# Kernel tuning notes

Hardware: AMD Instinct MI355X
Metric: run time of the kernel (lower is better)

Reference implementation:

```python
import jax, jax.numpy as jnp
import numpy as np


def conv1x1(x, w, b):
    # x: [B,Ci,H,W], w: [Co,Ci,1,1], b: [Co]
    return jnp.einsum('bihw,oi->bohw', x, w[:, :, 0, 0]) + b[None, :, None, None]


def guide_nn(x, w1, b1, w2, b2):
    h = jax.nn.relu(conv1x1(x, w1, b1))
    return jnp.tanh(conv1x1(h, w2, b2))


def trilinear_slice(grid, gx, gy, gz):
    # grid: [B,C,D,Gh,Gw]; gx,gy,gz: [B,H,W] in ~[-1,1]
    B, C, D, Gh, Gw = grid.shape
    fx = jnp.clip((gx + 1.0) * 0.5 * (Gw - 1), 0.0, Gw - 1)
    fy = jnp.clip((gy + 1.0) * 0.5 * (Gh - 1), 0.0, Gh - 1)
    fz = jnp.clip((gz + 1.0) * 0.5 * (D - 1), 0.0, D - 1)
    x0 = jnp.floor(fx).astype(jnp.int32); x1 = jnp.minimum(x0 + 1, Gw - 1)
    y0 = jnp.floor(fy).astype(jnp.int32); y1 = jnp.minimum(y0 + 1, Gh - 1)
    z0 = jnp.floor(fz).astype(jnp.int32); z1 = jnp.minimum(z0 + 1, D - 1)
    wx = (fx - x0)[:, None]; wy = (fy - y0)[:, None]; wz = (fz - z0)[:, None]

    gather = jax.vmap(lambda g, zi, yi, xi: g[:, zi, yi, xi])  # -> [B,C,H,W]

    out = (
        gather(grid, z0, y0, x0) * (1 - wz) * (1 - wy) * (1 - wx)
        + gather(grid, z0, y0, x1) * (1 - wz) * (1 - wy) * wx
        + gather(grid, z0, y1, x0) * (1 - wz) * wy * (1 - wx)
        + gather(grid, z0, y1, x1) * (1 - wz) * wy * wx
        + gather(grid, z1, y0, x0) * wz * (1 - wy) * (1 - wx)
        + gather(grid, z1, y0, x1) * wz * (1 - wy) * wx
        + gather(grid, z1, y1, x0) * wz * wy * (1 - wx)
        + gather(grid, z1, y1, x1) * wz * wy * wx
    )
    return out


def slicing(grid, guide):
    # guide: [B,1,H,W] (single-channel context map)
    B, c, H, W = guide.shape
    x = (jnp.arange(W, dtype=guide.dtype) - W / 2) / (W / 2)
    y = (jnp.arange(H, dtype=guide.dtype) - H / 2) / (H / 2)
    yy, xx = jnp.meshgrid(y, x, indexing='ij')
    gx = jnp.broadcast_to(xx[None], (B, H, W))
    gy = jnp.broadcast_to(yy[None], (B, H, W))
    gz = guide[:, 0]
    return trilinear_slice(grid, gx, gy, gz)


def apply_coefficent(x, coeff):
    # x: [B,Ci,H,W]; coeff: [B,Co,Ci+1,H,W] -> per-pixel affine
    ci = x.shape[1]
    return jnp.einsum('boihw,bihw->bohw', coeff[:, :, :ci], x) + coeff[:, :, ci]


def setup_inputs() -> dict:
    key = jax.random.key(0)
    ks = jax.random.split(key, 12)
    B, H, W = 8, 512, 512
    D, Gh, Gw = 8, 16, 16
    inp = {
        'src': jax.random.uniform(ks[0], (B, 3, H, W), jnp.float32),
        'grid1': jax.random.normal(ks[1], (B, 32, D, Gh, Gw), jnp.float32),
        'grid2': jax.random.normal(ks[2], (B, 27, D, Gh, Gw), jnp.float32),
        'w1': jax.random.normal(ks[3], (16, 3, 1, 1), jnp.float32) * 0.1,
        'b1': jnp.zeros((16,), jnp.float32),
        'w2': jax.random.normal(ks[4], (1, 16, 1, 1), jnp.float32) * 0.1,
        'b2': jnp.zeros((1,), jnp.float32),
        'w3': jax.random.normal(ks[5], (16, 8, 1, 1), jnp.float32) * 0.1,
        'b3': jnp.zeros((16,), jnp.float32),
        'w4': jax.random.normal(ks[6], (1, 16, 1, 1), jnp.float32) * 0.1,
        'b4': jnp.zeros((1,), jnp.float32),
    }
    return inp


def reference(src, grid1, grid2, w1, b1, w2, b2, w3, b3, w4, b4):
    B, _, H, W = src.shape
    context_map = guide_nn(src, w1, b1, w2, b2)            # [B,1,H,W]
    coeff1 = slicing(grid1, context_map)                    # [B,32,H,W]
    coeff1_split = jnp.transpose(coeff1.reshape(B, 4, 8, H, W), (0, 2, 1, 3, 4))  # [B,8,4,H,W]
    hidden = jax.nn.relu(apply_coefficent(src, coeff1_split))  # [B,8,H,W]
    context_map2 = guide_nn(hidden, w3, b3, w4, b4)         # [B,1,H,W]
    coeff2 = slicing(grid2, context_map2)                   # [B,27,H,W]
    coeff2_split = jnp.transpose(coeff2.reshape(B, 9, 3, H, W), (0, 2, 1, 3, 4))  # [B,3,9,H,W]
    out = apply_coefficent(hidden, coeff2_split)            # [B,3,H,W]
    return out
```

## Files before the change

### kernel.cpp

```cpp
#include <hip/hip_runtime.h>
#include <math.h>

#define BATCH 8
#define IMH 512
#define IMW 512
#define HWSZ (IMH * IMW)
#define CH 32
#define CPADH 40
#define L_CELLS (16 * 8)
#define LSLOTH (L_CELLS * CPADH)

typedef _Float16 h1;
typedef _Float16 h2 __attribute__((ext_vector_type(2)));

union V16 {
    uint4 u;
    h2 h[4];
};
union V8 {
    uint2 u;
    h2 h[2];
};

__device__ __forceinline__ float fast_tanh(float x) {
    float e = __expf(2.0f * x);
    return fmaf(-2.0f, __builtin_amdgcn_rcpf(e + 1.0f), 1.0f);
}
__device__ __forceinline__ unsigned packh(float a, float b) {
    h2 v;
    v[0] = (h1)a;
    v[1] = (h1)b;
    return __builtin_bit_cast(unsigned, v);
}
__device__ __forceinline__ h2 ash2(unsigned u) { return __builtin_bit_cast(h2, u); }
__device__ __forceinline__ h2 pkmax0(h2 v) { return __builtin_elementwise_max(v, (h2)(h1)0.0f); }


__global__ __launch_bounds__(256) void transpose_both(const float* __restrict__ g1,
                                                      const float* __restrict__ g2,
                                                      h1* __restrict__ t1,
                                                      h1* __restrict__ t2,
                                                      unsigned* __restrict__ wpk,
                                                      const float* __restrict__ w1,
                                                      const float* __restrict__ b1,
                                                      const float* __restrict__ w2,
                                                      const float* __restrict__ w3,
                                                      const float* __restrict__ b3,
                                                      const float* __restrict__ w4) {
    int idx = blockIdx.x * 256 + threadIdx.x;
    if (idx < 524288) {
        int x = idx & 15, y = (idx >> 4) & 15, z = (idx >> 8) & 7;
        int c = (idx >> 11) & 31, b = idx >> 16;
        t1[((((b * 16 + y) * 16 + x) * 8 + z) << 5) + c] = (h1)g1[idx];
    } else if (idx < 966656) {
        int j = idx - 524288;
        int x = j & 15, y = (j >> 4) & 15, z = (j >> 8) & 7;
        int r = j >> 11;
        int c = r % 27, b = r / 27;
        t2[((((b * 16 + y) * 16 + x) * 8 + z) << 5) + c] = (h1)g2[j];
    } else {
        int k = idx - 966656;
        int cell = k / 5, p = k - cell * 5;
        t2[(cell << 5) + 27 + p] = (h1)0.0f;
    }
    if (blockIdx.x == 4095) {
        int t = threadIdx.x;
        if (t < 24) {
            int i = t >> 3, n = t & 7;
            wpk[t] = packh(w1[2 * n * 3 + i], w1[(2 * n + 1) * 3 + i]);
        } else if (t < 32) {
            int n = t - 24;
            wpk[t] = packh(b1[2 * n], b1[2 * n + 1]);
        } else if (t < 40) {
            int n = t - 32;
            wpk[t] = packh(w2[2 * n], w2[2 * n + 1]);
        } else if (t < 104) {
            int k = t - 40;
            int n = k >> 3, i = k & 7;
            wpk[t] = packh(w3[2 * n * 8 + i], w3[(2 * n + 1) * 8 + i]);
        } else if (t < 112) {
            int n = t - 104;
            wpk[t] = packh(w4[2 * n], w4[2 * n + 1]);
        } else if (t < 120) {
            int n = t - 112;
            wpk[t] = packh(b3[2 * n], b3[2 * n + 1]);
        }
    }
}

template <bool TR>
__global__ __launch_bounds__(512, 8) void fused9(
    const float* __restrict__ src,
    const void* __restrict__ g1p,
    const void* __restrict__ g2p,
    const unsigned* __restrict__ wpk,
    const float* __restrict__ w1, const float* __restrict__ b1,
    const float* __restrict__ w2, const float* __restrict__ b2,
    const float* __restrict__ w3, const float* __restrict__ b3,
    const float* __restrict__ w4, const float* __restrict__ b4,
    float* __restrict__ out) {
    __shared__ __align__(16) h1 L1h[LSLOTH];
    __shared__ __align__(16) h1 L2h[LSLOTH];

    int tid = threadIdx.x;
    int h = blockIdx.x & 511;
    int b = blockIdx.x >> 9;

    float fy = (float)h * (15.0f / 512.0f);
    int y0 = (int)fy;
    float wy = fy - (float)y0;

    const float* sbase = src + (size_t)b * 3 * HWSZ + (size_t)h * IMW;
    float s0 = sbase[tid];
    float s1 = sbase[HWSZ + tid];
    float s2 = sbase[2 * HWSZ + tid];

    if (TR) {
        h2 wyh = (h2)(h1)wy;
        const uint4* p1 = (const uint4*)g1p + ((size_t)b * 16 + y0) * 512;
        const uint4* p2 = (const uint4*)g2p + ((size_t)b * 16 + y0) * 512;
        int g = tid & 3, cell = tid >> 2;
        V16 v0, v1, r0;
        v0.u = p1[tid];
        v1.u = p1[tid + 512];
#pragma unroll
        for (int k = 0; k < 4; ++k) r0.h[k] = v0.h[k] + (v1.h[k] - v0.h[k]) * wyh;
        *(uint4*)&L1h[cell * CPADH + 8 * g] = r0.u;
        V16 u0, u1, r1;
        u0.u = p2[tid];
        u1.u = p2[tid + 512];
#pragma unroll
        for (int k = 0; k < 4; ++k) r1.h[k] = u0.h[k] + (u1.h[k] - u0.h[k]) * wyh;
        *(uint4*)&L2h[cell * CPADH + 8 * g] = r1.u;
    } else {
        const float* g1f = (const float*)g1p;
        const float* g2f = (const float*)g2p;
        for (int t = tid; t < L_CELLS * CH; t += 512) {
            int c = t & 31, cell = t >> 5;
            int z = cell & 7, xj = cell >> 3;
            size_t o0 = ((((size_t)b * 32 + c) * 8 + z) * 16 + y0) * 16 + xj;
            float v0 = g1f[o0], v1 = g1f[o0 + 16];
            L1h[cell * CPADH + c] = (h1)fmaf(wy, v1 - v0, v0);
        }
        for (int t = tid; t < L_CELLS * CH; t += 512) {
            int c = t & 31, cell = t >> 5;
            int z = cell & 7, xj = cell >> 3;
            float v = 0.0f;
            if (c < 27) {
                size_t o0 = ((((size_t)b * 27 + c) * 8 + z) * 16 + y0) * 16 + xj;
                v = fmaf(wy, g2f[o0 + 16] - g2f[o0], g2f[o0]);
            }
            L2h[cell * CPADH + c] = (h1)v;
        }
    }
    __syncthreads();

    float* obase = out + (size_t)b * 3 * HWSZ + (size_t)h * IMW;
    int w = tid;

    float acc;
    h2 s0h, s1h, s2h;
    if constexpr (TR) {
        s0h = (h2)(h1)s0;
        s1h = (h2)(h1)s1;
        s2h = (h2)(h1)s2;
        h2 A;
#pragma unroll
        for (int n = 0; n < 8; ++n) {
            h2 t = ash2(wpk[24 + n]);
            t += s0h * ash2(wpk[n]);
            t += s1h * ash2(wpk[8 + n]);
            t += s2h * ash2(wpk[16 + n]);
            t = pkmax0(t);
            if (n == 0) A = t * ash2(wpk[32]);
            else        A += t * ash2(wpk[32 + n]);
        }
        acc = b2[0] + (float)A[0] + (float)A[1];
    } else {
        acc = b2[0];
#pragma unroll
        for (int j = 0; j < 16; ++j) {
            float t = fmaf(w1[j * 3 + 0], s0,
                      fmaf(w1[j * 3 + 1], s1,
                      fmaf(w1[j * 3 + 2], s2, b1[j])));
            acc = fmaf(w2[j], fmaxf(t, 0.0f), acc);
        }
    }
    float fz = fmaf(fast_tanh(acc), 3.5f, 3.5f);
    fz = fminf(fmaxf(fz, 0.0f), 7.0f);
    int z0 = min((int)fz, 6);
    float wz = fz - (float)z0;

    float fx = (float)w * (15.0f / 512.0f);
    int x0 = (int)fx;
    float wx = fx - (float)x0;
    int a00 = (x0 * 8 + z0) * CPADH;

    float w11v = wx * wz;
    float w10v = wx - w11v;
    float w01v = wz - w11v;
    float w00v = 1.0f - wx - wz + w11v;
    h2 W00 = (h2)(h1)w00v, W01 = (h2)(h1)w01v, W10 = (h2)(h1)w10v, W11 = (h2)(h1)w11v;

    const uint4* p00 = (const uint4*)&L1h[a00];
    const uint4* p01 = (const uint4*)&L1h[a00 + CPADH];
    const uint4* p10 = (const uint4*)&L1h[a00 + 8 * CPADH];
    const uint4* p11 = (const uint4*)&L1h[a00 + 9 * CPADH];
    h2 c1h[16];
#pragma unroll
    for (int j = 0; j < 4; ++j) {
        V16 A, B, C, D;
        A.u = p00[j];
        B.u = p01[j];
        C.u = p10[j];
        D.u = p11[j];
#pragma unroll
        for (int k = 0; k < 4; ++k)
            c1h[j * 4 + k] = A.h[k] * W00 + B.h[k] * W01 + C.h[k] * W10 + D.h[k] * W11;
    }

    h2 hidh[4];
    float hidf[8];
    if constexpr (TR) {
#pragma unroll
        for (int n = 0; n < 4; ++n) {
            h2 t = c1h[12 + n];
            t += c1h[n] * s0h;
            t += c1h[4 + n] * s1h;
            t += c1h[8 + n] * s2h;
            hidh[n] = pkmax0(t);
        }
    } else {
#pragma unroll
        for (int o = 0; o < 8; ++o) {
            float t = fmaf((float)c1h[o >> 1][o & 1], s0,
                      fmaf((float)c1h[(8 + o) >> 1][o & 1], s1,
                      fmaf((float)c1h[(16 + o) >> 1][o & 1], s2,
                           (float)c1h[(24 + o) >> 1][o & 1])));
            hidf[o] = fmaxf(t, 0.0f);
        }
    }

    float acc2;
    if constexpr (TR) {
        h2 hs[8];
#pragma unroll
        for (int n = 0; n < 4; ++n) {
            hs[2 * n]     = (h2)hidh[n][0];
            hs[2 * n + 1] = (h2)hidh[n][1];
        }
        h2 A;
#pragma unroll
        for (int n = 0; n < 8; ++n) {
            h2 t = ash2(wpk[112 + n]);
#pragma unroll
            for (int i = 0; i < 8; ++i) t += hs[i] * ash2(wpk[40 + n * 8 + i]);
            t = pkmax0(t);
            if (n == 0) A = t * ash2(wpk[104]);
            else        A += t * ash2(wpk[104 + n]);
        }
        acc2 = b4[0] + (float)A[0] + (float)A[1];
#pragma unroll
        for (int n = 0; n < 4; ++n) {
            hidf[2 * n]     = (float)hidh[n][0];
            hidf[2 * n + 1] = (float)hidh[n][1];
        }
    } else {
        acc2 = b4[0];
#pragma unroll
        for (int j = 0; j < 16; ++j) {
            float t = b3[j];
#pragma unroll
            for (int i = 0; i < 8; ++i) t = fmaf(w3[j * 8 + i], hidf[i], t);
            acc2 = fmaf(w4[j], fmaxf(t, 0.0f), acc2);
        }
    }
    float fz2 = fmaf(fast_tanh(acc2), 3.5f, 3.5f);
    fz2 = fminf(fmaxf(fz2, 0.0f), 7.0f);
    int z0b = min((int)fz2, 6);
    float wz2 = fz2 - (float)z0b;

    int a00b = (x0 * 8 + z0b) * CPADH;
    float u11 = wx * wz2;
    float u10 = wx - u11;
    float u01 = wz2 - u11;
    float u00 = 1.0f - wx - wz2 + u11;
    h2 U00 = (h2)(h1)u00, U01 = (h2)(h1)u01, U10 = (h2)(h1)u10, U11 = (h2)(h1)u11;

    const uint4* q00 = (const uint4*)&L2h[a00b];
    const uint4* q01 = (const uint4*)&L2h[a00b + CPADH];
    const uint4* q10 = (const uint4*)&L2h[a00b + 8 * CPADH];
    const uint4* q11 = (const uint4*)&L2h[a00b + 9 * CPADH];
    h2 c2h[14];
#pragma unroll
    for (int j = 0; j < 3; ++j) {
        V16 A, B, C, D;
        A.u = q00[j];
        B.u = q01[j];
        C.u = q10[j];
        D.u = q11[j];
#pragma unroll
        for (int k = 0; k < 4; ++k)
            c2h[j * 4 + k] = A.h[k] * U00 + B.h[k] * U01 + C.h[k] * U10 + D.h[k] * U11;
    }
    {
        V8 A, B, C, D;
        A.u = *(const uint2*)&L2h[a00b + 24];
        B.u = *(const uint2*)&L2h[a00b + CPADH + 24];
        C.u = *(const uint2*)&L2h[a00b + 8 * CPADH + 24];
        D.u = *(const uint2*)&L2h[a00b + 9 * CPADH + 24];
#pragma unroll
        for (int k = 0; k < 2; ++k)
            c2h[12 + k] = A.h[k] * U00 + B.h[k] * U01 + C.h[k] * U10 + D.h[k] * U11;
    }

#pragma unroll
    for (int o = 0; o < 3; ++o) {
        float t = (float)c2h[(24 + o) >> 1][(24 + o) & 1];
#pragma unroll
        for (int i = 0; i < 8; ++i) {
            int c = i * 3 + o;
            t = fmaf((float)c2h[c >> 1][c & 1], hidf[i], t);
        }
        obase[(size_t)o * HWSZ + w] = t;
    }
}

extern "C" void kernel_launch(void* const* d_in, const int* in_sizes, int n_in,
                              void* d_out, int out_size, void* d_ws, size_t ws_size,
                              hipStream_t stream) {
    const float* src   = (const float*)d_in[0];
    const float* grid1 = (const float*)d_in[1];
    const float* grid2 = (const float*)d_in[2];
    const float* w1 = (const float*)d_in[3];
    const float* b1 = (const float*)d_in[4];
    const float* w2 = (const float*)d_in[5];
    const float* b2 = (const float*)d_in[6];
    const float* w3 = (const float*)d_in[7];
    const float* b3 = (const float*)d_in[8];
    const float* w4 = (const float*)d_in[9];
    const float* b4 = (const float*)d_in[10];
    float* out = (float*)d_out;

    const size_t t_elems = (size_t)BATCH * 2048 * CH;
    const size_t ws_needed = 2 * t_elems * sizeof(h1) + 512;

    const int nblk = BATCH * IMH;

    if (ws_size >= ws_needed) {
        h1* t1 = (h1*)d_ws;
        h1* t2 = t1 + t_elems;
        unsigned* wpk = (unsigned*)(t2 + t_elems);
        transpose_both<<<4096, 256, 0, stream>>>(grid1, grid2, t1, t2, wpk,
                                                 w1, b1, w2, w3, b3, w4);
        fused9<true><<<nblk, 512, 0, stream>>>(
            src, t1, t2, wpk, w1, b1, w2, b2, w3, b3, w4, b4, out);
    } else {
        fused9<false><<<nblk, 512, 0, stream>>>(
            src, grid1, grid2, nullptr, w1, b1, w2, b2, w3, b3, w4, b4, out);
    }
}
```

Measured before the change: 119.7 us.

## Process four rows per block with double-buffered LDS slabs and prefetch

Each block now handles four consecutive image rows instead of one, cutting the grid to a quarter of its former size. Grid-slab loads and the next row's source pixels are issued before the current row is computed, so global-load latency can overlap with compute, and the slab goes into an alternating LDS buffer. This removes per-block launch and prologue cost and the separate load-then-sync stall for each row. In exchange it doubles shared-memory use, lowers the occupancy hint from 8 to 6, keeps more prefetched values in registers, and leaves fewer blocks to spread across CUs.

```diff
diff --git a/kernel.cpp b/kernel.cpp
--- a/kernel.cpp
+++ b/kernel.cpp
@@ -9,6 +9,7 @@
 #define CPADH 40
 #define L_CELLS (16 * 8)
 #define LSLOTH (L_CELLS * CPADH)
+#define ROWS 4
 
 typedef _Float16 h1;
 typedef _Float16 h2 __attribute__((ext_vector_type(2)));
@@ -89,7 +90,7 @@
 }
 
 template <bool TR>
-__global__ __launch_bounds__(512, 8) void fused9(
+__global__ __launch_bounds__(512, 6) void fused10(
     const float* __restrict__ src,
     const void* __restrict__ g1p,
     const void* __restrict__ g2p,
@@ -99,230 +100,279 @@
     const float* __restrict__ w3, const float* __restrict__ b3,
     const float* __restrict__ w4, const float* __restrict__ b4,
     float* __restrict__ out) {
-    __shared__ __align__(16) h1 L1h[LSLOTH];
-    __shared__ __align__(16) h1 L2h[LSLOTH];
+    __shared__ __align__(16) h1 L1h[2][LSLOTH];
+    __shared__ __align__(16) h1 L2h[2][LSLOTH];
 
     int tid = threadIdx.x;
-    int h = blockIdx.x & 511;
-    int b = blockIdx.x >> 9;
-
-    float fy = (float)h * (15.0f / 512.0f);
-    int y0 = (int)fy;
-    float wy = fy - (float)y0;
-
-    const float* sbase = src + (size_t)b * 3 * HWSZ + (size_t)h * IMW;
-    float s0 = sbase[tid];
-    float s1 = sbase[HWSZ + tid];
-    float s2 = sbase[2 * HWSZ + tid];
-
-    if (TR) {
-        h2 wyh = (h2)(h1)wy;
-        const uint4* p1 = (const uint4*)g1p + ((size_t)b * 16 + y0) * 512;
-        const uint4* p2 = (const uint4*)g2p + ((size_t)b * 16 + y0) * 512;
-        int g = tid & 3, cell = tid >> 2;
+    int b = blockIdx.x >> 7;
+    int h0 = (blockIdx.x & 127) << 2;
+
+    const float* sb0 = src + (size_t)b * 3 * HWSZ;
+    float* ob0 = out + (size_t)b * 3 * HWSZ;
+    int g = tid & 3, cell = tid >> 2;
+
+    uint4 va, vb, ua, ub;
+    float s0c, s1c, s2c, s0n, s1n, s2n;
+
+    auto issue_loads = [&](int r) {
+        float fyr = (float)(h0 + r) * (15.0f / 512.0f);
+        int y0r = (int)fyr;
+        const uint4* p1 = (const uint4*)g1p + ((size_t)b * 16 + y0r) * 512;
+        const uint4* p2 = (const uint4*)g2p + ((size_t)b * 16 + y0r) * 512;
+        va = p1[tid];
+        vb = p1[tid + 512];
+        ua = p2[tid];
+        ub = p2[tid + 512];
+    };
+    auto write_slab = [&](int r, int bi) {
+        float fyr = (float)(h0 + r) * (15.0f / 512.0f);
+        int y0r = (int)fyr;
+        h2 wyh = (h2)(h1)(fyr - (float)y0r);
         V16 v0, v1, r0;
-        v0.u = p1[tid];
-        v1.u = p1[tid + 512];
+        v0.u = va;
+        v1.u = vb;
 #pragma unroll
         for (int k = 0; k < 4; ++k) r0.h[k] = v0.h[k] + (v1.h[k] - v0.h[k]) * wyh;
-        *(uint4*)&L1h[cell * CPADH + 8 * g] = r0.u;
+        *(uint4*)&L1h[bi][cell * CPADH + 8 * g] = r0.u;
         V16 u0, u1, r1;
-        u0.u = p2[tid];
-        u1.u = p2[tid + 512];
+        u0.u = ua;
+        u1.u = ub;
 #pragma unroll
         for (int k = 0; k < 4; ++k) r1.h[k] = u0.h[k] + (u1.h[k] - u0.h[k]) * wyh;
-        *(uint4*)&L2h[cell * CPADH + 8 * g] = r1.u;
-    } else {
-        const float* g1f = (const float*)g1p;
-        const float* g2f = (const float*)g2p;
-        for (int t = tid; t < L_CELLS * CH; t += 512) {
-            int c = t & 31, cell = t >> 5;
-            int z = cell & 7, xj = cell >> 3;
-            size_t o0 = ((((size_t)b * 32 + c) * 8 + z) * 16 + y0) * 16 + xj;
-            float v0 = g1f[o0], v1 = g1f[o0 + 16];
-            L1h[cell * CPADH + c] = (h1)fmaf(wy, v1 - v0, v0);
-        }
-        for (int t = tid; t < L_CELLS * CH; t += 512) {
-            int c = t & 31, cell = t >> 5;
-            int z = cell & 7, xj = cell >> 3;
-            float v = 0.0f;
-            if (c < 27) {
-                size_t o0 = ((((size_t)b * 27 + c) * 8 + z) * 16 + y0) * 16 + xj;
-                v = fmaf(wy, g2f[o0 + 16] - g2f[o0], g2f[o0]);
-            }
-            L2h[cell * CPADH + c] = (h1)v;
-        }
+        *(uint4*)&L2h[bi][cell * CPADH + 8 * g] = r1.u;
+    };
+
+    if constexpr (TR) {
+        const float* sb = sb0 + (size_t)h0 * IMW;
+        s0c = sb[tid];
+        s1c = sb[HWSZ + tid];
+        s2c = sb[2 * HWSZ + tid];
+        issue_loads(0);
+        write_slab(0, 0);
     }
-    __syncthreads();
-
-    float* obase = out + (size_t)b * 3 * HWSZ + (size_t)h * IMW;
-    int w = tid;
-
-    float acc;
-    h2 s0h, s1h, s2h;
-    if constexpr (TR) {
-        s0h = (h2)(h1)s0;
-        s1h = (h2)(h1)s1;
-        s2h = (h2)(h1)s2;
-        h2 A;
-#pragma unroll
-        for (int n = 0; n < 8; ++n) {
-            h2 t = ash2(wpk[24 + n]);
-            t += s0h * ash2(wpk[n]);
-            t += s1h * ash2(wpk[8 + n]);
-            t += s2h * ash2(wpk[16 + n]);
-            t = pkmax0(t);
-            if (n == 0) A = t * ash2(wpk[32]);
-            else        A += t * ash2(wpk[32 + n]);
-        }
-        acc = b2[0] + (float)A[0] + (float)A[1];
-    } else {
-        acc = b2[0];
-#pragma unroll
-        for (int j = 0; j < 16; ++j) {
-            float t = fmaf(w1[j * 3 + 0], s0,
-                      fmaf(w1[j * 3 + 1], s1,
-                      fmaf(w1[j * 3 + 2], s2, b1[j])));
-            acc = fmaf(w2[j], fmaxf(t, 0.0f), acc);
-        }
-    }
-    float fz = fmaf(fast_tanh(acc), 3.5f, 3.5f);
-    fz = fminf(fmaxf(fz, 0.0f), 7.0f);
-    int z0 = min((int)fz, 6);
-    float wz = fz - (float)z0;
-
-    float fx = (float)w * (15.0f / 512.0f);
-    int x0 = (int)fx;
-    float wx = fx - (float)x0;
-    int a00 = (x0 * 8 + z0) * CPADH;
-
-    float w11v = wx * wz;
-    float w10v = wx - w11v;
-    float w01v = wz - w11v;
-    float w00v = 1.0f - wx - wz + w11v;
-    h2 W00 = (h2)(h1)w00v, W01 = (h2)(h1)w01v, W10 = (h2)(h1)w10v, W11 = (h2)(h1)w11v;
-
-    const uint4* p00 = (const uint4*)&L1h[a00];
-    const uint4* p01 = (const uint4*)&L1h[a00 + CPADH];
-    const uint4* p10 = (const uint4*)&L1h[a00 + 8 * CPADH];
-    const uint4* p11 = (const uint4*)&L1h[a00 + 9 * CPADH];
-    h2 c1h[16];
-#pragma unroll
-    for (int j = 0; j < 4; ++j) {
-        V16 A, B, C, D;
-        A.u = p00[j];
-        B.u = p01[j];
-        C.u = p10[j];
-        D.u = p11[j];
-#pragma unroll
-        for (int k = 0; k < 4; ++k)
-            c1h[j * 4 + k] = A.h[k] * W00 + B.h[k] * W01 + C.h[k] * W10 + D.h[k] * W11;
-    }
-
-    h2 hidh[4];
-    float hidf[8];
-    if constexpr (TR) {
-#pragma unroll
-        for (int n = 0; n < 4; ++n) {
-            h2 t = c1h[12 + n];
-            t += c1h[n] * s0h;
-            t += c1h[4 + n] * s1h;
-            t += c1h[8 + n] * s2h;
-            hidh[n] = pkmax0(t);
-        }
-    } else {
-#pragma unroll
-        for (int o = 0; o < 8; ++o) {
-            float t = fmaf((float)c1h[o >> 1][o & 1], s0,
-                      fmaf((float)c1h[(8 + o) >> 1][o & 1], s1,
-                      fmaf((float)c1h[(16 + o) >> 1][o & 1], s2,
-                           (float)c1h[(24 + o) >> 1][o & 1])));
-            hidf[o] = fmaxf(t, 0.0f);
-        }
-    }
-
-    float acc2;
-    if constexpr (TR) {
-        h2 hs[8];
-#pragma unroll
-        for (int n = 0; n < 4; ++n) {
-            hs[2 * n]     = (h2)hidh[n][0];
-            hs[2 * n + 1] = (h2)hidh[n][1];
-        }
-        h2 A;
-#pragma unroll
-        for (int n = 0; n < 8; ++n) {
-            h2 t = ash2(wpk[112 + n]);
-#pragma unroll
-            for (int i = 0; i < 8; ++i) t += hs[i] * ash2(wpk[40 + n * 8 + i]);
-            t = pkmax0(t);
-            if (n == 0) A = t * ash2(wpk[104]);
-            else        A += t * ash2(wpk[104 + n]);
-        }
-        acc2 = b4[0] + (float)A[0] + (float)A[1];
-#pragma unroll
-        for (int n = 0; n < 4; ++n) {
-            hidf[2 * n]     = (float)hidh[n][0];
-            hidf[2 * n + 1] = (float)hidh[n][1];
-        }
-    } else {
-        acc2 = b4[0];
-#pragma unroll
-        for (int j = 0; j < 16; ++j) {
-            float t = b3[j];
-#pragma unroll
-            for (int i = 0; i < 8; ++i) t = fmaf(w3[j * 8 + i], hidf[i], t);
-            acc2 = fmaf(w4[j], fmaxf(t, 0.0f), acc2);
-        }
-    }
-    float fz2 = fmaf(fast_tanh(acc2), 3.5f, 3.5f);
-    fz2 = fminf(fmaxf(fz2, 0.0f), 7.0f);
-    int z0b = min((int)fz2, 6);
-    float wz2 = fz2 - (float)z0b;
-
-    int a00b = (x0 * 8 + z0b) * CPADH;
-    float u11 = wx * wz2;
-    float u10 = wx - u11;
-    float u01 = wz2 - u11;
-    float u00 = 1.0f - wx - wz2 + u11;
-    h2 U00 = (h2)(h1)u00, U01 = (h2)(h1)u01, U10 = (h2)(h1)u10, U11 = (h2)(h1)u11;
-
-    const uint4* q00 = (const uint4*)&L2h[a00b];
-    const uint4* q01 = (const uint4*)&L2h[a00b + CPADH];
-    const uint4* q10 = (const uint4*)&L2h[a00b + 8 * CPADH];
-    const uint4* q11 = (const uint4*)&L2h[a00b + 9 * CPADH];
-    h2 c2h[14];
-#pragma unroll
-    for (int j = 0; j < 3; ++j) {
-        V16 A, B, C, D;
-        A.u = q00[j];
-        B.u = q01[j];
-        C.u = q10[j];
-        D.u = q11[j];
-#pragma unroll
-        for (int k = 0; k < 4; ++k)
-            c2h[j * 4 + k] = A.h[k] * U00 + B.h[k] * U01 + C.h[k] * U10 + D.h[k] * U11;
-    }
-    {
-        V8 A, B, C, D;
-        A.u = *(const uint2*)&L2h[a00b + 24];
-        B.u = *(const uint2*)&L2h[a00b + CPADH + 24];
-        C.u = *(const uint2*)&L2h[a00b + 8 * CPADH + 24];
-        D.u = *(const uint2*)&L2h[a00b + 9 * CPADH + 24];
-#pragma unroll
-        for (int k = 0; k < 2; ++k)
-            c2h[12 + k] = A.h[k] * U00 + B.h[k] * U01 + C.h[k] * U10 + D.h[k] * U11;
-    }
-
-#pragma unroll
-    for (int o = 0; o < 3; ++o) {
-        float t = (float)c2h[(24 + o) >> 1][(24 + o) & 1];
-#pragma unroll
-        for (int i = 0; i < 8; ++i) {
-            int c = i * 3 + o;
-            t = fmaf((float)c2h[c >> 1][c & 1], hidf[i], t);
-        }
-        obase[(size_t)o * HWSZ + w] = t;
+
+#pragma unroll
+    for (int r = 0; r < ROWS; ++r) {
+        int hr = h0 + r;
+        if constexpr (TR) {
+            if (r < ROWS - 1) {
+                issue_loads(r + 1);
+                const float* sb = sb0 + (size_t)(hr + 1) * IMW;
+                s0n = sb[tid];
+                s1n = sb[HWSZ + tid];
+                s2n = sb[2 * HWSZ + tid];
+            }
+        } else {
+            if (r > 0) __syncthreads();
+            float fyr = (float)hr * (15.0f / 512.0f);
+            int y0r = (int)fyr;
+            float wyr = fyr - (float)y0r;
+            const float* g1f = (const float*)g1p;
+            const float* g2f = (const float*)g2p;
+            for (int t = tid; t < L_CELLS * CH; t += 512) {
+                int c = t & 31, cl = t >> 5;
+                int z = cl & 7, xj = cl >> 3;
+                size_t o0 = ((((size_t)b * 32 + c) * 8 + z) * 16 + y0r) * 16 + xj;
+                float v0 = g1f[o0], v1 = g1f[o0 + 16];
+                L1h[r & 1][cl * CPADH + c] = (h1)fmaf(wyr, v1 - v0, v0);
+            }
+            for (int t = tid; t < L_CELLS * CH; t += 512) {
+                int c = t & 31, cl = t >> 5;
+                int z = cl & 7, xj = cl >> 3;
+                float v = 0.0f;
+                if (c < 27) {
+                    size_t o0 = ((((size_t)b * 27 + c) * 8 + z) * 16 + y0r) * 16 + xj;
+                    v = fmaf(wyr, g2f[o0 + 16] - g2f[o0], g2f[o0]);
+                }
+                L2h[r & 1][cl * CPADH + c] = (h1)v;
+            }
+            const float* sb = sb0 + (size_t)hr * IMW;
+            s0c = sb[tid];
+            s1c = sb[HWSZ + tid];
+            s2c = sb[2 * HWSZ + tid];
+        }
+        __syncthreads();
+
+        const h1* B1 = L1h[r & 1];
+        const h1* B2 = L2h[r & 1];
+        float* obase = ob0 + (size_t)hr * IMW;
+        int w = tid;
+
+        float acc;
+        h2 s0h, s1h, s2h;
+        if constexpr (TR) {
+            s0h = (h2)(h1)s0c;
+            s1h = (h2)(h1)s1c;
+            s2h = (h2)(h1)s2c;
+            h2 A;
+#pragma unroll
+            for (int n = 0; n < 8; ++n) {
+                h2 t = ash2(wpk[24 + n]);
+                t += s0h * ash2(wpk[n]);
+                t += s1h * ash2(wpk[8 + n]);
+                t += s2h * ash2(wpk[16 + n]);
+                t = pkmax0(t);
+                if (n == 0) A = t * ash2(wpk[32]);
+                else        A += t * ash2(wpk[32 + n]);
+            }
+            acc = b2[0] + (float)A[0] + (float)A[1];
+        } else {
+            acc = b2[0];
+#pragma unroll
+            for (int j = 0; j < 16; ++j) {
+                float t = fmaf(w1[j * 3 + 0], s0c,
+                          fmaf(w1[j * 3 + 1], s1c,
+                          fmaf(w1[j * 3 + 2], s2c, b1[j])));
+                acc = fmaf(w2[j], fmaxf(t, 0.0f), acc);
+            }
+        }
+        float fz = fmaf(fast_tanh(acc), 3.5f, 3.5f);
+        fz = fminf(fmaxf(fz, 0.0f), 7.0f);
+        int z0 = min((int)fz, 6);
+        float wz = fz - (float)z0;
+
+        float fx = (float)w * (15.0f / 512.0f);
+        int x0 = (int)fx;
+        float wx = fx - (float)x0;
+        int a00 = (x0 * 8 + z0) * CPADH;
+
+        float w11v = wx * wz;
+        float w10v = wx - w11v;
+        float w01v = wz - w11v;
+        float w00v = 1.0f - wx - wz + w11v;
+        h2 W00 = (h2)(h1)w00v, W01 = (h2)(h1)w01v, W10 = (h2)(h1)w10v, W11 = (h2)(h1)w11v;
+
+        const uint4* p00 = (const uint4*)&B1[a00];
+        const uint4* p01 = (const uint4*)&B1[a00 + CPADH];
+        const uint4* p10 = (const uint4*)&B1[a00 + 8 * CPADH];
+        const uint4* p11 = (const uint4*)&B1[a00 + 9 * CPADH];
+        h2 c1h[16];
+#pragma unroll
+        for (int j = 0; j < 4; ++j) {
+            V16 A, B, C, D;
+            A.u = p00[j];
+            B.u = p01[j];
+            C.u = p10[j];
+            D.u = p11[j];
+#pragma unroll
+            for (int k = 0; k < 4; ++k)
+                c1h[j * 4 + k] = A.h[k] * W00 + B.h[k] * W01 + C.h[k] * W10 + D.h[k] * W11;
+        }
+
+        h2 hidh[4];
+        float hidf[8];
+        if constexpr (TR) {
+#pragma unroll
+            for (int n = 0; n < 4; ++n) {
+                h2 t = c1h[12 + n];
+                t += c1h[n] * s0h;
+                t += c1h[4 + n] * s1h;
+                t += c1h[8 + n] * s2h;
+                hidh[n] = pkmax0(t);
+            }
+        } else {
+#pragma unroll
+            for (int o = 0; o < 8; ++o) {
+                float t = fmaf((float)c1h[o >> 1][o & 1], s0c,
+                          fmaf((float)c1h[(8 + o) >> 1][o & 1], s1c,
+                          fmaf((float)c1h[(16 + o) >> 1][o & 1], s2c,
+                               (float)c1h[(24 + o) >> 1][o & 1])));
+                hidf[o] = fmaxf(t, 0.0f);
+            }
+        }
+
+        float acc2;
+        if constexpr (TR) {
+            h2 hs[8];
+#pragma unroll
+            for (int n = 0; n < 4; ++n) {
+                hs[2 * n]     = (h2)hidh[n][0];
+                hs[2 * n + 1] = (h2)hidh[n][1];
+            }
+            h2 A;
+#pragma unroll
+            for (int n = 0; n < 8; ++n) {
+                h2 t = ash2(wpk[112 + n]);
+#pragma unroll
+                for (int i = 0; i < 8; ++i) t += hs[i] * ash2(wpk[40 + n * 8 + i]);
+                t = pkmax0(t);
+                if (n == 0) A = t * ash2(wpk[104]);
+                else        A += t * ash2(wpk[104 + n]);
+            }
+            acc2 = b4[0] + (float)A[0] + (float)A[1];
+#pragma unroll
+            for (int n = 0; n < 4; ++n) {
+                hidf[2 * n]     = (float)hidh[n][0];
+                hidf[2 * n + 1] = (float)hidh[n][1];
+            }
+        } else {
+            acc2 = b4[0];
+#pragma unroll
+            for (int j = 0; j < 16; ++j) {
+                float t = b3[j];
+#pragma unroll
+                for (int i = 0; i < 8; ++i) t = fmaf(w3[j * 8 + i], hidf[i], t);
+                acc2 = fmaf(w4[j], fmaxf(t, 0.0f), acc2);
+            }
+        }
+        float fz2 = fmaf(fast_tanh(acc2), 3.5f, 3.5f);
+        fz2 = fminf(fmaxf(fz2, 0.0f), 7.0f);
+        int z0b = min((int)fz2, 6);
+        float wz2 = fz2 - (float)z0b;
+
+        int a00b = (x0 * 8 + z0b) * CPADH;
+        float u11 = wx * wz2;
+        float u10 = wx - u11;
+        float u01 = wz2 - u11;
+        float u00 = 1.0f - wx - wz2 + u11;
+        h2 U00 = (h2)(h1)u00, U01 = (h2)(h1)u01, U10 = (h2)(h1)u10, U11 = (h2)(h1)u11;
+
+        const uint4* q00 = (const uint4*)&B2[a00b];
+        const uint4* q01 = (const uint4*)&B2[a00b + CPADH];
+        const uint4* q10 = (const uint4*)&B2[a00b + 8 * CPADH];
+        const uint4* q11 = (const uint4*)&B2[a00b + 9 * CPADH];
+        h2 c2h[14];
+#pragma unroll
+        for (int j = 0; j < 3; ++j) {
+            V16 A, B, C, D;
+            A.u = q00[j];
+            B.u = q01[j];
+            C.u = q10[j];
+            D.u = q11[j];
+#pragma unroll
+            for (int k = 0; k < 4; ++k)
+                c2h[j * 4 + k] = A.h[k] * U00 + B.h[k] * U01 + C.h[k] * U10 + D.h[k] * U11;
+        }
+        {
+            V8 A, B, C, D;
+            A.u = *(const uint2*)&B2[a00b + 24];
+            B.u = *(const uint2*)&B2[a00b + CPADH + 24];
+            C.u = *(const uint2*)&B2[a00b + 8 * CPADH + 24];
+            D.u = *(const uint2*)&B2[a00b + 9 * CPADH + 24];
+#pragma unroll
+            for (int k = 0; k < 2; ++k)
+                c2h[12 + k] = A.h[k] * U00 + B.h[k] * U01 + C.h[k] * U10 + D.h[k] * U11;
+        }
+
+#pragma unroll
+        for (int o = 0; o < 3; ++o) {
+            float t = (float)c2h[(24 + o) >> 1][(24 + o) & 1];
+#pragma unroll
+            for (int i = 0; i < 8; ++i) {
+                int c = i * 3 + o;
+                t = fmaf((float)c2h[c >> 1][c & 1], hidf[i], t);
+            }
+            obase[(size_t)o * HWSZ + w] = t;
+        }
+
+        if constexpr (TR) {
+            if (r < ROWS - 1) {
+                write_slab(r + 1, (r + 1) & 1);
+                s0c = s0n;
+                s1c = s1n;
+                s2c = s2n;
+            }
+        }
     }
 }
 
@@ -345,7 +395,7 @@
     const size_t t_elems = (size_t)BATCH * 2048 * CH;
     const size_t ws_needed = 2 * t_elems * sizeof(h1) + 512;
 
-    const int nblk = BATCH * IMH;
+    const int nblk = BATCH * IMH / ROWS;
 
     if (ws_size >= ws_needed) {
         h1* t1 = (h1*)d_ws;
@@ -353,10 +403,10 @@
         unsigned* wpk = (unsigned*)(t2 + t_elems);
         transpose_both<<<4096, 256, 0, stream>>>(grid1, grid2, t1, t2, wpk,
                                                  w1, b1, w2, w3, b3, w4);
-        fused9<true><<<nblk, 512, 0, stream>>>(
+        fused10<true><<<nblk, 512, 0, stream>>>(
             src, t1, t2, wpk, w1, b1, w2, b2, w3, b3, w4, b4, out);
     } else {
-        fused9<false><<<nblk, 512, 0, stream>>>(
+        fused10<false><<<nblk, 512, 0, stream>>>(
             src, grid1, grid2, nullptr, w1, b1, w2, b2, w3, b3, w4, b4, out);
     }
 }
```

Result: slower. 127.4 us (+6.4%).

## Drop grid transpose kernel; load fp32 grids directly with float4 in fused kernel

Applied to the files above, without the earlier changes.

Removes the separate transpose/pack pre-kernel and has each block read the original fp32 grids with vectorized float4 loads, converting to half, lerping in y and writing the cell-major LDS layout itself. The guide MLPs go back to fp32 FMAs with scalar weights instead of packed-half weights, and the occupancy hint drops from 8 to 6. This is meant to remove one launch and the workspace round-trip. In exchange each of the 4096 blocks re-reads grid rows from global memory, and the MLPs now do more fp32 arithmetic per pixel.

```diff
diff --git a/kernel.cpp b/kernel.cpp
--- a/kernel.cpp
+++ b/kernel.cpp
@@ -5,7 +5,6 @@
 #define IMH 512
 #define IMW 512
 #define HWSZ (IMH * IMW)
-#define CH 32
 #define CPADH 40
 #define L_CELLS (16 * 8)
 #define LSLOTH (L_CELLS * CPADH)
@@ -26,74 +25,12 @@
     float e = __expf(2.0f * x);
     return fmaf(-2.0f, __builtin_amdgcn_rcpf(e + 1.0f), 1.0f);
 }
-__device__ __forceinline__ unsigned packh(float a, float b) {
-    h2 v;
-    v[0] = (h1)a;
-    v[1] = (h1)b;
-    return __builtin_bit_cast(unsigned, v);
-}
-__device__ __forceinline__ h2 ash2(unsigned u) { return __builtin_bit_cast(h2, u); }
 __device__ __forceinline__ h2 pkmax0(h2 v) { return __builtin_elementwise_max(v, (h2)(h1)0.0f); }
 
-
-__global__ __launch_bounds__(256) void transpose_both(const float* __restrict__ g1,
-                                                      const float* __restrict__ g2,
-                                                      h1* __restrict__ t1,
-                                                      h1* __restrict__ t2,
-                                                      unsigned* __restrict__ wpk,
-                                                      const float* __restrict__ w1,
-                                                      const float* __restrict__ b1,
-                                                      const float* __restrict__ w2,
-                                                      const float* __restrict__ w3,
-                                                      const float* __restrict__ b3,
-                                                      const float* __restrict__ w4) {
-    int idx = blockIdx.x * 256 + threadIdx.x;
-    if (idx < 524288) {
-        int x = idx & 15, y = (idx >> 4) & 15, z = (idx >> 8) & 7;
-        int c = (idx >> 11) & 31, b = idx >> 16;
-        t1[((((b * 16 + y) * 16 + x) * 8 + z) << 5) + c] = (h1)g1[idx];
-    } else if (idx < 966656) {
-        int j = idx - 524288;
-        int x = j & 15, y = (j >> 4) & 15, z = (j >> 8) & 7;
-        int r = j >> 11;
-        int c = r % 27, b = r / 27;
-        t2[((((b * 16 + y) * 16 + x) * 8 + z) << 5) + c] = (h1)g2[j];
-    } else {
-        int k = idx - 966656;
-        int cell = k / 5, p = k - cell * 5;
-        t2[(cell << 5) + 27 + p] = (h1)0.0f;
-    }
-    if (blockIdx.x == 4095) {
-        int t = threadIdx.x;
-        if (t < 24) {
-            int i = t >> 3, n = t & 7;
-            wpk[t] = packh(w1[2 * n * 3 + i], w1[(2 * n + 1) * 3 + i]);
-        } else if (t < 32) {
-            int n = t - 24;
-            wpk[t] = packh(b1[2 * n], b1[2 * n + 1]);
-        } else if (t < 40) {
-            int n = t - 32;
-            wpk[t] = packh(w2[2 * n], w2[2 * n + 1]);
-        } else if (t < 104) {
-            int k = t - 40;
-            int n = k >> 3, i = k & 7;
-            wpk[t] = packh(w3[2 * n * 8 + i], w3[(2 * n + 1) * 8 + i]);
-        } else if (t < 112) {
-            int n = t - 104;
-            wpk[t] = packh(w4[2 * n], w4[2 * n + 1]);
-        } else if (t < 120) {
-            int n = t - 112;
-            wpk[t] = packh(b3[2 * n], b3[2 * n + 1]);
-        }
-    }
-}
-
-template <bool TR>
-__global__ __launch_bounds__(512, 8) void fused9(
+__global__ __launch_bounds__(512, 6) void fused11(
     const float* __restrict__ src,
-    const void* __restrict__ g1p,
-    const void* __restrict__ g2p,
-    const unsigned* __restrict__ wpk,
+    const float* __restrict__ g1,
+    const float* __restrict__ g2,
     const float* __restrict__ w1, const float* __restrict__ b1,
     const float* __restrict__ w2, const float* __restrict__ b2,
     const float* __restrict__ w3, const float* __restrict__ b3,
@@ -115,76 +52,62 @@
     float s1 = sbase[HWSZ + tid];
     float s2 = sbase[2 * HWSZ + tid];
 
-    if (TR) {
+    {
         h2 wyh = (h2)(h1)wy;
-        const uint4* p1 = (const uint4*)g1p + ((size_t)b * 16 + y0) * 512;
-        const uint4* p2 = (const uint4*)g2p + ((size_t)b * 16 + y0) * 512;
-        int g = tid & 3, cell = tid >> 2;
-        V16 v0, v1, r0;
-        v0.u = p1[tid];
-        v1.u = p1[tid + 512];
-#pragma unroll
-        for (int k = 0; k < 4; ++k) r0.h[k] = v0.h[k] + (v1.h[k] - v0.h[k]) * wyh;
-        *(uint4*)&L1h[cell * CPADH + 8 * g] = r0.u;
-        V16 u0, u1, r1;
-        u0.u = p2[tid];
-        u1.u = p2[tid + 512];
-#pragma unroll
-        for (int k = 0; k < 4; ++k) r1.h[k] = u0.h[k] + (u1.h[k] - u0.h[k]) * wyh;
-        *(uint4*)&L2h[cell * CPADH + 8 * g] = r1.u;
-    } else {
-        const float* g1f = (const float*)g1p;
-        const float* g2f = (const float*)g2p;
-        for (int t = tid; t < L_CELLS * CH; t += 512) {
-            int c = t & 31, cell = t >> 5;
-            int z = cell & 7, xj = cell >> 3;
-            size_t o0 = ((((size_t)b * 32 + c) * 8 + z) * 16 + y0) * 16 + xj;
-            float v0 = g1f[o0], v1 = g1f[o0 + 16];
-            L1h[cell * CPADH + c] = (h1)fmaf(wy, v1 - v0, v0);
-        }
-        for (int t = tid; t < L_CELLS * CH; t += 512) {
-            int c = t & 31, cell = t >> 5;
-            int z = cell & 7, xj = cell >> 3;
-            float v = 0.0f;
-            if (c < 27) {
-                size_t o0 = ((((size_t)b * 27 + c) * 8 + z) * 16 + y0) * 16 + xj;
-                v = fmaf(wy, g2f[o0 + 16] - g2f[o0], g2f[o0]);
+        if (tid < 480) {
+            bool isg1 = tid < 256;
+            int v = isg1 ? tid : tid - 256;
+            int x4 = v & 3, z = (v >> 2) & 7, cg = v >> 5;
+            const float4* gp = isg1 ? (const float4*)g1 : (const float4*)g2;
+            size_t base = (isg1 ? (size_t)b * 16384 : (size_t)b * 13824)
+                        + (size_t)(cg * 4) * 512 + z * 64 + y0 * 4 + x4;
+            int cmax = isg1 ? 32 : 27;
+            h1 hv[4][2][4];
+#pragma unroll
+            for (int cc = 0; cc < 4; ++cc) {
+                if (cg * 4 + cc < cmax) {
+                    float4 v0 = gp[base + (size_t)cc * 512];
+                    float4 v1 = gp[base + (size_t)cc * 512 + 4];
+                    hv[cc][0][0] = (h1)v0.x; hv[cc][0][1] = (h1)v0.y;
+                    hv[cc][0][2] = (h1)v0.z; hv[cc][0][3] = (h1)v0.w;
+                    hv[cc][1][0] = (h1)v1.x; hv[cc][1][1] = (h1)v1.y;
+                    hv[cc][1][2] = (h1)v1.z; hv[cc][1][3] = (h1)v1.w;
+                } else {
+#pragma unroll
+                    for (int yy = 0; yy < 2; ++yy)
+#pragma unroll
+                        for (int xi = 0; xi < 4; ++xi) hv[cc][yy][xi] = (h1)0.0f;
+                }
             }
-            L2h[cell * CPADH + c] = (h1)v;
+            h1* dst = isg1 ? L1h : L2h;
+#pragma unroll
+            for (int xi = 0; xi < 4; ++xi) {
+                int cell = (x4 * 4 + xi) * 8 + z;
+                h2 a01, b01, a23, b23;
+                a01[0] = hv[0][0][xi]; a01[1] = hv[1][0][xi];
+                b01[0] = hv[0][1][xi]; b01[1] = hv[1][1][xi];
+                a23[0] = hv[2][0][xi]; a23[1] = hv[3][0][xi];
+                b23[0] = hv[2][1][xi]; b23[1] = hv[3][1][xi];
+                V8 r;
+                r.h[0] = a01 + (b01 - a01) * wyh;
+                r.h[1] = a23 + (b23 - a23) * wyh;
+                *(uint2*)&dst[cell * CPADH + cg * 4] = r.u;
+            }
         }
     }
     __syncthreads();
 
     float* obase = out + (size_t)b * 3 * HWSZ + (size_t)h * IMW;
     int w = tid;
-
-    float acc;
-    h2 s0h, s1h, s2h;
-    if constexpr (TR) {
-        s0h = (h2)(h1)s0;
-        s1h = (h2)(h1)s1;
-        s2h = (h2)(h1)s2;
-        h2 A;
-#pragma unroll
-        for (int n = 0; n < 8; ++n) {
-            h2 t = ash2(wpk[24 + n]);
-            t += s0h * ash2(wpk[n]);
-            t += s1h * ash2(wpk[8 + n]);
-            t += s2h * ash2(wpk[16 + n]);
-            t = pkmax0(t);
-            if (n == 0) A = t * ash2(wpk[32]);
-            else        A += t * ash2(wpk[32 + n]);
-        }
-        acc = b2[0] + (float)A[0] + (float)A[1];
-    } else {
-        acc = b2[0];
-#pragma unroll
-        for (int j = 0; j < 16; ++j) {
-            float t = fmaf(w1[j * 3 + 0], s0,
-                      fmaf(w1[j * 3 + 1], s1,
-                      fmaf(w1[j * 3 + 2], s2, b1[j])));
-            acc = fmaf(w2[j], fmaxf(t, 0.0f), acc);
-        }
+    h2 s0h = (h2)(h1)s0, s1h = (h2)(h1)s1, s2h = (h2)(h1)s2;
+
+    float acc = b2[0];
+#pragma unroll
+    for (int j = 0; j < 16; ++j) {
+        float t = fmaf(w1[j * 3 + 0], s0,
+                  fmaf(w1[j * 3 + 1], s1,
+                  fmaf(w1[j * 3 + 2], s2, b1[j])));
+        acc = fmaf(w2[j], fmaxf(t, 0.0f), acc);
     }
     float fz = fmaf(fast_tanh(acc), 3.5f, 3.5f);
     fz = fminf(fmaxf(fz, 0.0f), 7.0f);
@@ -219,61 +142,25 @@
             c1h[j * 4 + k] = A.h[k] * W00 + B.h[k] * W01 + C.h[k] * W10 + D.h[k] * W11;
     }
 
-    h2 hidh[4];
     float hidf[8];
-    if constexpr (TR) {
-#pragma unroll
-        for (int n = 0; n < 4; ++n) {
-            h2 t = c1h[12 + n];
-            t += c1h[n] * s0h;
-            t += c1h[4 + n] * s1h;
-            t += c1h[8 + n] * s2h;
-            hidh[n] = pkmax0(t);
-        }
-    } else {
-#pragma unroll
-        for (int o = 0; o < 8; ++o) {
-            float t = fmaf((float)c1h[o >> 1][o & 1], s0,
-                      fmaf((float)c1h[(8 + o) >> 1][o & 1], s1,
-                      fmaf((float)c1h[(16 + o) >> 1][o & 1], s2,
-                           (float)c1h[(24 + o) >> 1][o & 1])));
-            hidf[o] = fmaxf(t, 0.0f);
-        }
-    }
-
-    float acc2;
-    if constexpr (TR) {
-        h2 hs[8];
-#pragma unroll
-        for (int n = 0; n < 4; ++n) {
-            hs[2 * n]     = (h2)hidh[n][0];
-            hs[2 * n + 1] = (h2)hidh[n][1];
-        }
-        h2 A;
-#pragma unroll
-        for (int n = 0; n < 8; ++n) {
-            h2 t = ash2(wpk[112 + n]);
-#pragma unroll
-            for (int i = 0; i < 8; ++i) t += hs[i] * ash2(wpk[40 + n * 8 + i]);
-            t = pkmax0(t);
-            if (n == 0) A = t * ash2(wpk[104]);
-            else        A += t * ash2(wpk[104 + n]);
-        }
-        acc2 = b4[0] + (float)A[0] + (float)A[1];
-#pragma unroll
-        for (int n = 0; n < 4; ++n) {
-            hidf[2 * n]     = (float)hidh[n][0];
-            hidf[2 * n + 1] = (float)hidh[n][1];
-        }
-    } else {
-        acc2 = b4[0];
-#pragma unroll
-        for (int j = 0; j < 16; ++j) {
-            float t = b3[j];
-#pragma unroll
-            for (int i = 0; i < 8; ++i) t = fmaf(w3[j * 8 + i], hidf[i], t);
-            acc2 = fmaf(w4[j], fmaxf(t, 0.0f), acc2);
-        }
+#pragma unroll
+    for (int n = 0; n < 4; ++n) {
+        h2 t = c1h[12 + n];
+        t += c1h[n] * s0h;
+        t += c1h[4 + n] * s1h;
+        t += c1h[8 + n] * s2h;
+        t = pkmax0(t);
+        hidf[2 * n]     = (float)t[0];
+        hidf[2 * n + 1] = (float)t[1];
+    }
+
+    float acc2 = b4[0];
+#pragma unroll
+    for (int j = 0; j < 16; ++j) {
+        float t = b3[j];
+#pragma unroll
+        for (int i = 0; i < 8; ++i) t = fmaf(w3[j * 8 + i], hidf[i], t);
+        acc2 = fmaf(w4[j], fmaxf(t, 0.0f), acc2);
     }
     float fz2 = fmaf(fast_tanh(acc2), 3.5f, 3.5f);
     fz2 = fminf(fmaxf(fz2, 0.0f), 7.0f);
@@ -342,21 +229,10 @@
     const float* b4 = (const float*)d_in[10];
     float* out = (float*)d_out;
 
-    const size_t t_elems = (size_t)BATCH * 2048 * CH;
-    const size_t ws_needed = 2 * t_elems * sizeof(h1) + 512;
+    (void)d_ws;
+    (void)ws_size;
 
     const int nblk = BATCH * IMH;
-
-    if (ws_size >= ws_needed) {
-        h1* t1 = (h1*)d_ws;
-        h1* t2 = t1 + t_elems;
-        unsigned* wpk = (unsigned*)(t2 + t_elems);
-        transpose_both<<<4096, 256, 0, stream>>>(grid1, grid2, t1, t2, wpk,
-                                                 w1, b1, w2, w3, b3, w4);
-        fused9<true><<<nblk, 512, 0, stream>>>(
-            src, t1, t2, wpk, w1, b1, w2, b2, w3, b3, w4, b4, out);
-    } else {
-        fused9<false><<<nblk, 512, 0, stream>>>(
-            src, grid1, grid2, nullptr, w1, b1, w2, b2, w3, b3, w4, b4, out);
-    }
+    fused11<<<nblk, 512, 0, stream>>>(
+        src, grid1, grid2, w1, b1, w2, b2, w3, b3, w4, b4, out);
 }
```

New measurement: 125.9 us. 1.05x slower.
